# Optimization experiments

Measured on AMD Instinct MI355X. Metric: run time of the kernel, lower is better.

## Reference

```python
import jax, jax.numpy as jnp
import numpy as np

D_MODEL, NUM_HEADS, D_HEAD = 1024, 16, 64
B, T = 2, 2048


def setup_inputs() -> dict:
    key = jax.random.key(0)
    ks = jax.random.split(key, 9)
    s_in = 1.0 / np.sqrt(D_MODEL)
    s_proj = 1.0 / np.sqrt(NUM_HEADS * D_HEAD)
    x = jax.random.normal(ks[0], (B, T, D_MODEL), dtype=jnp.float32)
    # stacked per-head projection weights (nn.Linear: y = x @ W.T + b -> store as [H, C, d_head])
    Wq = jax.random.uniform(ks[1], (NUM_HEADS, D_MODEL, D_HEAD), jnp.float32, -s_in, s_in)
    Wk = jax.random.uniform(ks[2], (NUM_HEADS, D_MODEL, D_HEAD), jnp.float32, -s_in, s_in)
    Wv = jax.random.uniform(ks[3], (NUM_HEADS, D_MODEL, D_HEAD), jnp.float32, -s_in, s_in)
    bq = jax.random.uniform(ks[4], (NUM_HEADS, D_HEAD), jnp.float32, -s_in, s_in)
    bk = jax.random.uniform(ks[5], (NUM_HEADS, D_HEAD), jnp.float32, -s_in, s_in)
    bv = jax.random.uniform(ks[6], (NUM_HEADS, D_HEAD), jnp.float32, -s_in, s_in)
    Wo = jax.random.uniform(ks[7], (NUM_HEADS * D_HEAD, D_MODEL), jnp.float32, -s_proj, s_proj)
    bo = jax.random.uniform(ks[8], (D_MODEL,), jnp.float32, -s_proj, s_proj)
    return {"x": x, "Wq": Wq, "Wk": Wk, "Wv": Wv, "bq": bq, "bk": bk, "bv": bv, "Wo": Wo, "bo": bo}


def reference(x, Wq, Wk, Wv, bq, bk, bv, Wo, bo):
    Bsz, Tlen, C = x.shape
    # per-head projections, vectorized over heads: [B, H, T, d_head]
    q = jnp.einsum('btc,hcd->bhtd', x, Wq) + bq[None, :, None, :]
    k = jnp.einsum('btc,hcd->bhtd', x, Wk) + bk[None, :, None, :]
    v = jnp.einsum('btc,hcd->bhtd', x, Wv) + bv[None, :, None, :]
    # NOTE: source scales by sqrt(C) = sqrt(d_model), not sqrt(d_head); no causal mask
    scores = jnp.einsum('bhtd,bhsd->bhts', q, k) / jnp.sqrt(jnp.asarray(C, x.dtype))
    attn = jax.nn.softmax(scores, axis=-1)
    out = jnp.einsum('bhts,bhsd->bhtd', attn, v)  # [B, H, T, d_head]
    # concat heads along feature dim: [B, T, H*d_head]
    out = jnp.transpose(out, (0, 2, 1, 3)).reshape(Bsz, Tlen, -1)
    return out @ Wo + bo
```

## Files before the change

kernel.cpp:

```cpp
#include <hip/hip_runtime.h>

typedef __bf16 bf16;
typedef __bf16 bf16x4 __attribute__((ext_vector_type(4)));
typedef __bf16 bf16x8 __attribute__((ext_vector_type(8)));
typedef float  f32x4  __attribute__((ext_vector_type(4)));

#define T_SEQ  2048
#define NHEAD  16
#define DHEAD  64
#define DMODEL 1024
#define MTOT   4096
#define L2E    1.4426950408889634f

static __device__ __forceinline__ f32x4 mfma16(bf16x8 a, bf16x8 b, f32x4 c) {
    return __builtin_amdgcn_mfma_f32_16x16x32_bf16(a, b, c, 0, 0, 0);
}

__global__ __launch_bounds__(256) void prep(
    const float* __restrict__ x,  bf16* __restrict__ xbf,
    const float* __restrict__ Wq, const float* __restrict__ Wk,
    const float* __restrict__ Wv, bf16* __restrict__ wt,
    const float* __restrict__ Wo, bf16* __restrict__ wot)
{
    __shared__ float t[64][68];
    const int bid = blockIdx.x, tid = threadIdx.x;

    if (bid < 2048) {
        const int i = bid * 256 + tid;
        const float4 a = ((const float4*)x)[i * 2];
        const float4 b = ((const float4*)x)[i * 2 + 1];
        bf16x8 v;
        v[0] = (bf16)a.x; v[1] = (bf16)a.y; v[2] = (bf16)a.z; v[3] = (bf16)a.w;
        v[4] = (bf16)b.x; v[5] = (bf16)b.y; v[6] = (bf16)b.z; v[7] = (bf16)b.w;
        ((bf16x8*)xbf)[i] = v;
        return;
    }

    const float* in; bf16* out;
    int R, Cc; long ib, ob; int r0, c0;
    if (bid < 2816) {
        int b2 = bid - 2048;
        int w = b2 >> 8, rem = b2 & 255;
        int rt = rem & 15, head = rem >> 4;
        in  = (w == 0 ? Wq : w == 1 ? Wk : Wv);
        out = wt + (size_t)w * 1024 * 1024;
        R = 1024; Cc = 64;
        ib = (long)head * 65536; ob = (long)head * 65536;
        r0 = rt * 64; c0 = 0;
    } else {
        int b3 = bid - 2816;
        in = Wo; out = wot;
        R = 1024; Cc = 1024;
        ib = 0; ob = 0;
        r0 = (b3 & 15) * 64; c0 = (b3 >> 4) * 64;
    }

#pragma unroll
    for (int i = 0; i < 4; ++i) {
        int idx = i * 256 + tid;
        int row = idx >> 4, cb = (idx & 15) * 4;
        float4 v = *(const float4*)&in[ib + (long)(r0 + row) * Cc + c0 + cb];
        t[row][cb + 0] = v.x; t[row][cb + 1] = v.y;
        t[row][cb + 2] = v.z; t[row][cb + 3] = v.w;
    }
    __syncthreads();
#pragma unroll
    for (int i = 0; i < 2; ++i) {
        int idx = i * 256 + tid;
        int row = idx >> 3, cb = (idx & 7) * 8;
        bf16x8 v;
#pragma unroll
        for (int j = 0; j < 8; ++j) v[j] = (bf16)t[cb + j][row];
        *(bf16x8*)&out[ob + (long)(c0 + row) * R + r0 + cb] = v;
    }
}

__global__ __launch_bounds__(256) void qkv_gemm(
    const bf16* __restrict__ x, const bf16* __restrict__ wt,
    const float* __restrict__ bq, const float* __restrict__ bk,
    const float* __restrict__ bv,
    bf16* __restrict__ qws, bf16* __restrict__ kws, bf16* __restrict__ vtws)
{
    __shared__ __align__(16) bf16 xs[128][72];
    __shared__ __align__(16) bf16 wsh[3][64][72];

    const int m0 = blockIdx.x * 128;
    const int h  = blockIdx.y;
    const int tid = threadIdx.x, wid = tid >> 6, lane = tid & 63;
    const int lr = lane & 15, lg = lane >> 4;

    const bf16* wbase[3];
#pragma unroll
    for (int w = 0; w < 3; ++w)
        wbase[w] = wt + ((size_t)(w * NHEAD + h)) * DHEAD * DMODEL;

    f32x4 acc[3][2][4];
#pragma unroll
    for (int w = 0; w < 3; ++w)
#pragma unroll
        for (int mi = 0; mi < 2; ++mi)
#pragma unroll
            for (int nt = 0; nt < 4; ++nt) acc[w][mi][nt] = (f32x4)0.0f;

    bf16x8 xr[4], wr[3][2];
#pragma unroll
    for (int i = 0; i < 4; ++i) {
        int idx = i * 256 + tid;
        int row = idx >> 3, cb = (idx & 7) * 8;
        xr[i] = *(const bf16x8*)&x[(size_t)(m0 + row) * DMODEL + cb];
    }
#pragma unroll
    for (int w = 0; w < 3; ++w)
#pragma unroll
        for (int i = 0; i < 2; ++i) {
            int idx = i * 256 + tid;
            int row = idx >> 3, cb = (idx & 7) * 8;
            wr[w][i] = *(const bf16x8*)&wbase[w][(size_t)row * DMODEL + cb];
        }

    for (int kt = 0; kt < 16; ++kt) {
        __syncthreads();
#pragma unroll
        for (int i = 0; i < 4; ++i) {
            int idx = i * 256 + tid;
            int row = idx >> 3, cb = (idx & 7) * 8;
            *(bf16x8*)&xs[row][cb] = xr[i];
        }
#pragma unroll
        for (int w = 0; w < 3; ++w)
#pragma unroll
            for (int i = 0; i < 2; ++i) {
                int idx = i * 256 + tid;
                int row = idx >> 3, cb = (idx & 7) * 8;
                *(bf16x8*)&wsh[w][row][cb] = wr[w][i];
            }
        __syncthreads();

        if (kt < 15) {
            const int kofs = (kt + 1) * 64;
#pragma unroll
            for (int i = 0; i < 4; ++i) {
                int idx = i * 256 + tid;
                int row = idx >> 3, cb = (idx & 7) * 8;
                xr[i] = *(const bf16x8*)&x[(size_t)(m0 + row) * DMODEL + kofs + cb];
            }
#pragma unroll
            for (int w = 0; w < 3; ++w)
#pragma unroll
                for (int i = 0; i < 2; ++i) {
                    int idx = i * 256 + tid;
                    int row = idx >> 3, cb = (idx & 7) * 8;
                    wr[w][i] = *(const bf16x8*)&wbase[w][(size_t)row * DMODEL + kofs + cb];
                }
        }

        bf16x8 af[2][2];
#pragma unroll
        for (int mi = 0; mi < 2; ++mi)
#pragma unroll
            for (int ks = 0; ks < 2; ++ks)
                af[mi][ks] = *(const bf16x8*)&xs[wid * 32 + mi * 16 + lr][ks * 32 + lg * 8];

#pragma unroll
        for (int w = 0; w < 3; ++w)
#pragma unroll
            for (int nt = 0; nt < 4; ++nt)
#pragma unroll
                for (int ks = 0; ks < 2; ++ks) {
                    bf16x8 bfr = *(const bf16x8*)&wsh[w][nt * 16 + lr][ks * 32 + lg * 8];
#pragma unroll
                    for (int mi = 0; mi < 2; ++mi)
                        acc[w][mi][nt] = mfma16(af[mi][ks], bfr, acc[w][mi][nt]);
                }
    }

    const float* bias[3] = { bq + h * DHEAD, bk + h * DHEAD, bv + h * DHEAD };
#pragma unroll
    for (int w = 0; w < 3; ++w)
#pragma unroll
        for (int nt = 0; nt < 4; ++nt) {
            int d = nt * 16 + lr;
            float bs = bias[w][d];
#pragma unroll
            for (int mi = 0; mi < 2; ++mi)
#pragma unroll
                for (int j = 0; j < 4; ++j) {
                    int mrow = m0 + wid * 32 + mi * 16 + lg * 4 + j;
                    int b = mrow >> 11, t = mrow & 2047;
                    float val = acc[w][mi][nt][j] + bs;
                    size_t bh = (size_t)b * NHEAD + h;
                    if (w == 0)
                        qws[(bh * T_SEQ + t) * DHEAD + d] = (bf16)val;
                    else if (w == 1)
                        kws[(bh * T_SEQ + t) * DHEAD + d] = (bf16)val;
                    else
                        vtws[(bh * DHEAD + d) * T_SEQ + t] = (bf16)val;
                }
        }
}

template<int S, bool PARTIAL>
__global__ __launch_bounds__(512, 4) void attn_split(
    const bf16* __restrict__ qws, const bf16* __restrict__ kws,
    const bf16* __restrict__ vtws,
    bf16* __restrict__ po, float* __restrict__ pml, bf16* __restrict__ aws)
{
    __shared__ __align__(16) bf16 kls[2][64][72];
    __shared__ __align__(16) bf16 vls[2][64][72];

    const int id = blockIdx.x;
    const int w  = (id & 7) * (32 * S) + (id >> 3);
    const int bh = w / (8 * S);
    const int rem = w - bh * (8 * S);
    const int qt = rem / S;
    const int sidx = rem - qt * S;
    const int t0 = (sidx * 32) / S, t1 = ((sidx + 1) * 32) / S;

    const int b = bh >> 4, h = bh & 15;
    const bf16* Q  = qws  + (size_t)bh * T_SEQ * DHEAD;
    const bf16* K  = kws  + (size_t)bh * T_SEQ * DHEAD;
    const bf16* Vt = vtws + (size_t)bh * DHEAD * T_SEQ;

    const int tid = threadIdx.x, wid = tid >> 6, lane = tid & 63;
    const int lr = lane & 15, lg = lane >> 4;

    const int srow = tid >> 3, scb = (tid & 7) * 8;
    const int sl = tid & 7;
    const int vcol = 32 * (sl >> 2) + 4 * (sl & 3);

    int q0[2];
    bf16x8 qf[2][2];
#pragma unroll
    for (int g = 0; g < 2; ++g) {
        q0[g] = qt * 256 + g * 128 + wid * 16;
#pragma unroll
        for (int ks = 0; ks < 2; ++ks) {
            bf16x8 v = *(const bf16x8*)&Q[(size_t)(q0[g] + lr) * DHEAD + ks * 32 + lg * 8];
#pragma unroll
            for (int j = 0; j < 8; ++j) v[j] = (bf16)((float)v[j] * 0.03125f);
            qf[g][ks] = v;
        }
    }

    f32x4 o[2][4];
#pragma unroll
    for (int g = 0; g < 2; ++g)
#pragma unroll
        for (int nt = 0; nt < 4; ++nt) o[g][nt] = (f32x4)0.0f;
    float mrun[2] = { -1e30f, -1e30f }, lrun[2] = { 0.f, 0.f };
    float m2c[2]  = { -1e30f * L2E, -1e30f * L2E };

    bf16x8 kr;
    bf16x4 va, vb;
    kr = *(const bf16x8*)&K[(size_t)(t0 * 64 + srow) * DHEAD + scb];
    va = *(const bf16x4*)&Vt[(size_t)srow * T_SEQ + t0 * 64 + vcol];
    vb = *(const bf16x4*)&Vt[(size_t)srow * T_SEQ + t0 * 64 + vcol + 16];
    *(bf16x8*)&kls[0][srow][scb] = kr;
    *(bf16x8*)&vls[0][srow][scb] = __builtin_shufflevector(va, vb, 0, 1, 2, 3, 4, 5, 6, 7);

    int cur = 0;
    for (int t = t0; t < t1; ++t) {
        __syncthreads();

        const bool more = (t + 1) < t1;
        if (more) {
            int kvn = (t + 1) * 64;
            kr = *(const bf16x8*)&K[(size_t)(kvn + srow) * DHEAD + scb];
            va = *(const bf16x4*)&Vt[(size_t)srow * T_SEQ + kvn + vcol];
            vb = *(const bf16x4*)&Vt[(size_t)srow * T_SEQ + kvn + vcol + 16];
        }

        f32x4 s[2][4];
        __builtin_amdgcn_s_setprio(1);
#pragma unroll
        for (int nt = 0; nt < 4; ++nt) {
            bf16x8 k0 = *(const bf16x8*)&kls[cur][nt * 16 + lr][0 + lg * 8];
            bf16x8 k1 = *(const bf16x8*)&kls[cur][nt * 16 + lr][32 + lg * 8];
#pragma unroll
            for (int g = 0; g < 2; ++g) {
                s[g][nt] = mfma16(k0, qf[g][0], (f32x4)0.0f);
                s[g][nt] = mfma16(k1, qf[g][1], s[g][nt]);
            }
        }
        __builtin_amdgcn_s_setprio(0);

        bf16x8 pf[2][2];
#pragma unroll
        for (int g = 0; g < 2; ++g) {
            float vm0 = fmaxf(fmaxf(s[g][0][0], s[g][0][1]), fmaxf(s[g][0][2], s[g][0][3]));
            float vm1 = fmaxf(fmaxf(s[g][1][0], s[g][1][1]), fmaxf(s[g][1][2], s[g][1][3]));
            float vm2 = fmaxf(fmaxf(s[g][2][0], s[g][2][1]), fmaxf(s[g][2][2], s[g][2][3]));
            float vm3 = fmaxf(fmaxf(s[g][3][0], s[g][3][1]), fmaxf(s[g][3][2], s[g][3][3]));
            float vm = fmaxf(fmaxf(vm0, vm1), fmaxf(vm2, vm3));

            const bool skip = __all(vm <= mrun[g] + 8.0f);
            if (!skip) {
                float vmr = fmaxf(vm, __shfl_xor(vm, 16));
                vmr = fmaxf(vmr, __shfl_xor(vmr, 32));
                float mnew = fmaxf(mrun[g], vmr);
                float alpha = __builtin_amdgcn_exp2f((mrun[g] - mnew) * L2E);
                lrun[g] *= alpha;
                mrun[g] = mnew;
                m2c[g] = mnew * L2E;
                float ab[4];
#pragma unroll
                for (int j = 0; j < 4; ++j) ab[j] = __shfl(alpha, lg * 4 + j);
#pragma unroll
                for (int nt = 0; nt < 4; ++nt)
#pragma unroll
                    for (int j = 0; j < 4; ++j) o[g][nt][j] *= ab[j];
            }

            const float m2 = m2c[g];
            float p[4][4];
            float rs = 0.f;
#pragma unroll
            for (int nt = 0; nt < 4; ++nt)
#pragma unroll
                for (int j = 0; j < 4; ++j) {
                    p[nt][j] = __builtin_amdgcn_exp2f(fmaf(s[g][nt][j], L2E, -m2));
                    rs += p[nt][j];
                }
            lrun[g] += rs;

#pragma unroll
            for (int ks = 0; ks < 2; ++ks) {
                bf16x8 pk;
#pragma unroll
                for (int j = 0; j < 4; ++j) {
                    pk[j]     = (bf16)p[2 * ks][j];
                    pk[j + 4] = (bf16)p[2 * ks + 1][j];
                }
                pf[g][ks] = pk;
            }
        }

        __builtin_amdgcn_s_setprio(1);
#pragma unroll
        for (int ks = 0; ks < 2; ++ks)
#pragma unroll
            for (int nt = 0; nt < 4; ++nt) {
                bf16x8 vf = *(const bf16x8*)&vls[cur][nt * 16 + lr][ks * 32 + lg * 8];
#pragma unroll
                for (int g = 0; g < 2; ++g)
                    o[g][nt] = mfma16(pf[g][ks], vf, o[g][nt]);
            }
        __builtin_amdgcn_s_setprio(0);

        if (more) {
            *(bf16x8*)&kls[cur ^ 1][srow][scb] = kr;
            *(bf16x8*)&vls[cur ^ 1][srow][scb] =
                __builtin_shufflevector(va, vb, 0, 1, 2, 3, 4, 5, 6, 7);
        }
        cur ^= 1;
    }

#pragma unroll
    for (int g = 0; g < 2; ++g) {
        float lrow = lrun[g];
        lrow += __shfl_xor(lrow, 16);
        lrow += __shfl_xor(lrow, 32);

        float linv[4];
#pragma unroll
        for (int j = 0; j < 4; ++j) linv[j] = 1.0f / __shfl(lrow, lg * 4 + j);

        if (PARTIAL) {
            const size_t pbase = (size_t)(sidx * 32 + bh) * T_SEQ * DHEAD;
#pragma unroll
            for (int nt = 0; nt < 4; ++nt) {
                int dcol = nt * 16 + lr;
#pragma unroll
                for (int j = 0; j < 4; ++j) {
                    int tq = q0[g] + lg * 4 + j;
                    po[pbase + (size_t)tq * DHEAD + dcol] = (bf16)(o[g][nt][j] * linv[j]);
                }
            }
            if (lg == 0) {
                size_t mlidx = ((size_t)(sidx * 32 + bh) * T_SEQ + (q0[g] + lr)) * 2;
                pml[mlidx]     = mrun[g];
                pml[mlidx + 1] = lrow;
            }
        } else {
            const size_t obase = ((size_t)b * T_SEQ) * DMODEL + (size_t)h * DHEAD;
#pragma unroll
            for (int nt = 0; nt < 4; ++nt) {
                int dcol = nt * 16 + lr;
#pragma unroll
                for (int j = 0; j < 4; ++j) {
                    int tq = q0[g] + lg * 4 + j;
                    aws[obase + (size_t)tq * DMODEL + dcol] = (bf16)(o[g][nt][j] * linv[j]);
                }
            }
        }
    }
}

template<int S>
__global__ __launch_bounds__(256) void attn_combine(
    const bf16* __restrict__ po, const float* __restrict__ pml,
    bf16* __restrict__ aws)
{
    const int g = blockIdx.x * 256 + threadIdx.x;
    const int r = g >> 3, dblk = g & 7;
    const int bh = r >> 11, tq = r & 2047;

    float ms[S], ls[S];
    float m = -1e30f;
#pragma unroll
    for (int s = 0; s < S; ++s) {
        float2 v = ((const float2*)pml)[(size_t)(s * 32 + bh) * T_SEQ + tq];
        ms[s] = v.x; ls[s] = v.y;
        m = fmaxf(m, ms[s]);
    }
    float L = 0.f, wgt[S];
#pragma unroll
    for (int s = 0; s < S; ++s) {
        wgt[s] = ls[s] * __builtin_amdgcn_exp2f((ms[s] - m) * L2E);
        L += wgt[s];
    }
    float inv = 1.0f / L;

    float acc[8];
#pragma unroll
    for (int j = 0; j < 8; ++j) acc[j] = 0.f;
#pragma unroll
    for (int s = 0; s < S; ++s) {
        bf16x8 ov = *(const bf16x8*)&po[((size_t)(s * 32 + bh) * T_SEQ + tq) * DHEAD + dblk * 8];
        float c = wgt[s] * inv;
#pragma unroll
        for (int j = 0; j < 8; ++j) acc[j] = fmaf(c, (float)ov[j], acc[j]);
    }
    bf16x8 out;
#pragma unroll
    for (int j = 0; j < 8; ++j) out[j] = (bf16)acc[j];

    const int b = bh >> 4, h = bh & 15;
    *(bf16x8*)&aws[((size_t)(b * T_SEQ + tq)) * DMODEL + h * DHEAD + dblk * 8] = out;
}

__global__ __launch_bounds__(256) void out_gemm(
    const bf16* __restrict__ a, const bf16* __restrict__ wot,
    const float* __restrict__ bo, float* __restrict__ out)
{
    __shared__ __align__(16) bf16 as[128][72];
    __shared__ __align__(16) bf16 wsh[128][72];

    const int m0 = blockIdx.x * 128, n0 = blockIdx.y * 128;
    const int tid = threadIdx.x, wid = tid >> 6, lane = tid & 63;
    const int lr = lane & 15, lg = lane >> 4;

    f32x4 acc[2][8];
#pragma unroll
    for (int mi = 0; mi < 2; ++mi)
#pragma unroll
        for (int nt = 0; nt < 8; ++nt) acc[mi][nt] = (f32x4)0.0f;

    bf16x8 ar[4], wr[4];
#pragma unroll
    for (int i = 0; i < 4; ++i) {
        int idx = i * 256 + tid;
        int row = idx >> 3, cb = (idx & 7) * 8;
        ar[i] = *(const bf16x8*)&a[(size_t)(m0 + row) * DMODEL + cb];
        wr[i] = *(const bf16x8*)&wot[(size_t)(n0 + row) * DMODEL + cb];
    }

    for (int kt = 0; kt < 16; ++kt) {
        __syncthreads();
#pragma unroll
        for (int i = 0; i < 4; ++i) {
            int idx = i * 256 + tid;
            int row = idx >> 3, cb = (idx & 7) * 8;
            *(bf16x8*)&as[row][cb]  = ar[i];
            *(bf16x8*)&wsh[row][cb] = wr[i];
        }
        __syncthreads();

        if (kt < 15) {
            const int kofs = (kt + 1) * 64;
#pragma unroll
            for (int i = 0; i < 4; ++i) {
                int idx = i * 256 + tid;
                int row = idx >> 3, cb = (idx & 7) * 8;
                ar[i] = *(const bf16x8*)&a[(size_t)(m0 + row) * DMODEL + kofs + cb];
                wr[i] = *(const bf16x8*)&wot[(size_t)(n0 + row) * DMODEL + kofs + cb];
            }
        }

        bf16x8 af[2][2];
#pragma unroll
        for (int mi = 0; mi < 2; ++mi)
#pragma unroll
            for (int ks = 0; ks < 2; ++ks)
                af[mi][ks] = *(const bf16x8*)&as[wid * 32 + mi * 16 + lr][ks * 32 + lg * 8];

#pragma unroll
        for (int nt = 0; nt < 8; ++nt)
#pragma unroll
            for (int ks = 0; ks < 2; ++ks) {
                bf16x8 bfr = *(const bf16x8*)&wsh[nt * 16 + lr][ks * 32 + lg * 8];
#pragma unroll
                for (int mi = 0; mi < 2; ++mi)
                    acc[mi][nt] = mfma16(af[mi][ks], bfr, acc[mi][nt]);
            }
    }

#pragma unroll
    for (int nt = 0; nt < 8; ++nt) {
        int n = n0 + nt * 16 + lr;
        float bs = bo[n];
#pragma unroll
        for (int mi = 0; mi < 2; ++mi)
#pragma unroll
            for (int j = 0; j < 4; ++j) {
                int m = m0 + wid * 32 + mi * 16 + lg * 4 + j;
                out[(size_t)m * DMODEL + n] = acc[mi][nt][j] + bs;
            }
    }
}

extern "C" void kernel_launch(void* const* d_in, const int* in_sizes, int n_in,
                              void* d_out, int out_size, void* d_ws, size_t ws_size,
                              hipStream_t stream)
{
    const float* x  = (const float*)d_in[0];
    const float* Wq = (const float*)d_in[1];
    const float* Wk = (const float*)d_in[2];
    const float* Wv = (const float*)d_in[3];
    const float* bq = (const float*)d_in[4];
    const float* bk = (const float*)d_in[5];
    const float* bv = (const float*)d_in[6];
    const float* Wo = (const float*)d_in[7];
    const float* bo = (const float*)d_in[8];
    float* out = (float*)d_out;

    const size_t M1 = (size_t)1024 * 1024;
    bf16* ws   = (bf16*)d_ws;
    bf16* xbf  = ws;
    bf16* qws  = ws + 4 * M1;
    bf16* kws  = qws + 4 * M1;
    bf16* vtws = kws + 4 * M1;
    bf16* wt   = vtws + 4 * M1;
    bf16* wot  = wt + 3 * M1;
    bf16* aws  = xbf;
    bf16* po   = wot + 1 * M1;

    const size_t BASE = 20 * M1 * 2;
    const size_t PER  = 4 * M1 * 2 + (size_t)65536 * 2 * 4;

    dim3 tb(256);
    prep<<<dim3(3072), tb, 0, stream>>>(x, xbf, Wq, Wk, Wv, wt, Wo, wot);
    qkv_gemm<<<dim3(MTOT / 128, NHEAD), tb, 0, stream>>>(xbf, wt, bq, bk, bv, qws, kws, vtws);

    if (ws_size >= BASE + 2 * PER) {
        float* pml = (float*)(po + 2 * 4 * M1);
        attn_split<2, true><<<dim3(512), dim3(512), 0, stream>>>(qws, kws, vtws, po, pml, aws);
        attn_combine<2><<<dim3(2048), tb, 0, stream>>>(po, pml, aws);
    } else {
        attn_split<1, false><<<dim3(256), dim3(512), 0, stream>>>(qws, kws, vtws, po, nullptr, aws);
    }

    out_gemm<<<dim3(MTOT / 128, DMODEL / 128), tb, 0, stream>>>(aws, wot, bo, out);
}
```

Measured before the change: 117.4 us.

## Compute softmax row sums via MFMA and shrink out-projection GEMM M-tile

In the attention kernel, the softmax denominator is now accumulated with an extra MFMA of the probability fragments against a ones vector. This replaces per-lane scalar adds and the cross-lane shuffle reductions, and the row sum arrives already in the output layout. The output-projection GEMM tile shrinks from 128 to 64 rows per block, doubling the block count to improve occupancy and CU coverage, at the cost of more weight-tile reloads. The MFMA-based sum adds matrix work per KV tile and accumulates from bf16-rounded probabilities.

```diff
diff --git a/kernel.cpp b/kernel.cpp
--- a/kernel.cpp
+++ b/kernel.cpp
@@ -228,6 +228,10 @@
     const int sl = tid & 7;
     const int vcol = 32 * (sl >> 2) + 4 * (sl & 3);
 
+    bf16x8 onesf;
+#pragma unroll
+    for (int j = 0; j < 8; ++j) onesf[j] = (bf16)1.0f;
+
     int q0[2];
     bf16x8 qf[2][2];
 #pragma unroll
@@ -242,12 +246,14 @@
         }
     }
 
-    f32x4 o[2][4];
-#pragma unroll
-    for (int g = 0; g < 2; ++g)
+    f32x4 o[2][4], lsum[2];
+#pragma unroll
+    for (int g = 0; g < 2; ++g) {
 #pragma unroll
         for (int nt = 0; nt < 4; ++nt) o[g][nt] = (f32x4)0.0f;
-    float mrun[2] = { -1e30f, -1e30f }, lrun[2] = { 0.f, 0.f };
+        lsum[g] = (f32x4)0.0f;
+    }
+    float mrun[2] = { -1e30f, -1e30f };
     float m2c[2]  = { -1e30f * L2E, -1e30f * L2E };
 
     bf16x8 kr;
@@ -299,13 +305,14 @@
                 vmr = fmaxf(vmr, __shfl_xor(vmr, 32));
                 float mnew = fmaxf(mrun[g], vmr);
                 float alpha = __builtin_amdgcn_exp2f((mrun[g] - mnew) * L2E);
-                lrun[g] *= alpha;
                 mrun[g] = mnew;
                 m2c[g] = mnew * L2E;
                 float ab[4];
 #pragma unroll
                 for (int j = 0; j < 4; ++j) ab[j] = __shfl(alpha, lg * 4 + j);
 #pragma unroll
+                for (int j = 0; j < 4; ++j) lsum[g][j] *= ab[j];
+#pragma unroll
                 for (int nt = 0; nt < 4; ++nt)
 #pragma unroll
                     for (int j = 0; j < 4; ++j) o[g][nt][j] *= ab[j];
@@ -313,15 +320,11 @@
 
             const float m2 = m2c[g];
             float p[4][4];
-            float rs = 0.f;
 #pragma unroll
             for (int nt = 0; nt < 4; ++nt)
 #pragma unroll
-                for (int j = 0; j < 4; ++j) {
+                for (int j = 0; j < 4; ++j)
                     p[nt][j] = __builtin_amdgcn_exp2f(fmaf(s[g][nt][j], L2E, -m2));
-                    rs += p[nt][j];
-                }
-            lrun[g] += rs;
 
 #pragma unroll
             for (int ks = 0; ks < 2; ++ks) {
@@ -337,7 +340,10 @@
 
         __builtin_amdgcn_s_setprio(1);
 #pragma unroll
-        for (int ks = 0; ks < 2; ++ks)
+        for (int ks = 0; ks < 2; ++ks) {
+#pragma unroll
+            for (int g = 0; g < 2; ++g)
+                lsum[g] = mfma16(pf[g][ks], onesf, lsum[g]);
 #pragma unroll
             for (int nt = 0; nt < 4; ++nt) {
                 bf16x8 vf = *(const bf16x8*)&vls[cur][nt * 16 + lr][ks * 32 + lg * 8];
@@ -345,6 +351,7 @@
                 for (int g = 0; g < 2; ++g)
                     o[g][nt] = mfma16(pf[g][ks], vf, o[g][nt]);
             }
+        }
         __builtin_amdgcn_s_setprio(0);
 
         if (more) {
@@ -357,13 +364,9 @@
 
 #pragma unroll
     for (int g = 0; g < 2; ++g) {
-        float lrow = lrun[g];
-        lrow += __shfl_xor(lrow, 16);
-        lrow += __shfl_xor(lrow, 32);
-
         float linv[4];
 #pragma unroll
-        for (int j = 0; j < 4; ++j) linv[j] = 1.0f / __shfl(lrow, lg * 4 + j);
+        for (int j = 0; j < 4; ++j) linv[j] = 1.0f / lsum[g][j];
 
         if (PARTIAL) {
             const size_t pbase = (size_t)(sidx * 32 + bh) * T_SEQ * DHEAD;
@@ -376,10 +379,18 @@
                     po[pbase + (size_t)tq * DHEAD + dcol] = (bf16)(o[g][nt][j] * linv[j]);
                 }
             }
-            if (lg == 0) {
-                size_t mlidx = ((size_t)(sidx * 32 + bh) * T_SEQ + (q0[g] + lr)) * 2;
-                pml[mlidx]     = mrun[g];
-                pml[mlidx + 1] = lrow;
+            {
+                int js = lr & 3;
+                float wv = lsum[g][0];
+                wv = (js == 1) ? lsum[g][1] : wv;
+                wv = (js == 2) ? lsum[g][2] : wv;
+                wv = (js == 3) ? lsum[g][3] : wv;
+                float lrow_q = __shfl(wv, 16 * (lr >> 2) + (lr & 3));
+                if (lg == 0) {
+                    size_t mlidx = ((size_t)(sidx * 32 + bh) * T_SEQ + (q0[g] + lr)) * 2;
+                    pml[mlidx]     = mrun[g];
+                    pml[mlidx + 1] = lrow_q;
+                }
             }
         } else {
             const size_t obase = ((size_t)b * T_SEQ) * DMODEL + (size_t)h * DHEAD;
@@ -443,65 +454,74 @@
     const bf16* __restrict__ a, const bf16* __restrict__ wot,
     const float* __restrict__ bo, float* __restrict__ out)
 {
-    __shared__ __align__(16) bf16 as[128][72];
+    __shared__ __align__(16) bf16 as[64][72];
     __shared__ __align__(16) bf16 wsh[128][72];
 
-    const int m0 = blockIdx.x * 128, n0 = blockIdx.y * 128;
+    const int m0 = blockIdx.x * 64, n0 = blockIdx.y * 128;
     const int tid = threadIdx.x, wid = tid >> 6, lane = tid & 63;
     const int lr = lane & 15, lg = lane >> 4;
 
-    f32x4 acc[2][8];
-#pragma unroll
-    for (int mi = 0; mi < 2; ++mi)
-#pragma unroll
-        for (int nt = 0; nt < 8; ++nt) acc[mi][nt] = (f32x4)0.0f;
-
-    bf16x8 ar[4], wr[4];
+    f32x4 acc[8];
+#pragma unroll
+    for (int nt = 0; nt < 8; ++nt) acc[nt] = (f32x4)0.0f;
+
+    bf16x8 ar[2], wr[4];
+#pragma unroll
+    for (int i = 0; i < 2; ++i) {
+        int idx = i * 256 + tid;
+        int row = idx >> 3, cb = (idx & 7) * 8;
+        ar[i] = *(const bf16x8*)&a[(size_t)(m0 + row) * DMODEL + cb];
+    }
 #pragma unroll
     for (int i = 0; i < 4; ++i) {
         int idx = i * 256 + tid;
         int row = idx >> 3, cb = (idx & 7) * 8;
-        ar[i] = *(const bf16x8*)&a[(size_t)(m0 + row) * DMODEL + cb];
         wr[i] = *(const bf16x8*)&wot[(size_t)(n0 + row) * DMODEL + cb];
     }
 
     for (int kt = 0; kt < 16; ++kt) {
         __syncthreads();
+#pragma unroll
+        for (int i = 0; i < 2; ++i) {
+            int idx = i * 256 + tid;
+            int row = idx >> 3, cb = (idx & 7) * 8;
+            *(bf16x8*)&as[row][cb] = ar[i];
+        }
 #pragma unroll
         for (int i = 0; i < 4; ++i) {
             int idx = i * 256 + tid;
             int row = idx >> 3, cb = (idx & 7) * 8;
-            *(bf16x8*)&as[row][cb]  = ar[i];
             *(bf16x8*)&wsh[row][cb] = wr[i];
         }
         __syncthreads();
 
         if (kt < 15) {
             const int kofs = (kt + 1) * 64;
+#pragma unroll
+            for (int i = 0; i < 2; ++i) {
+                int idx = i * 256 + tid;
+                int row = idx >> 3, cb = (idx & 7) * 8;
+                ar[i] = *(const bf16x8*)&a[(size_t)(m0 + row) * DMODEL + kofs + cb];
+            }
 #pragma unroll
             for (int i = 0; i < 4; ++i) {
                 int idx = i * 256 + tid;
                 int row = idx >> 3, cb = (idx & 7) * 8;
-                ar[i] = *(const bf16x8*)&a[(size_t)(m0 + row) * DMODEL + kofs + cb];
                 wr[i] = *(const bf16x8*)&wot[(size_t)(n0 + row) * DMODEL + kofs + cb];
             }
         }
 
-        bf16x8 af[2][2];
-#pragma unroll
-        for (int mi = 0; mi < 2; ++mi)
-#pragma unroll
-            for (int ks = 0; ks < 2; ++ks)
-                af[mi][ks] = *(const bf16x8*)&as[wid * 32 + mi * 16 + lr][ks * 32 + lg * 8];
+        bf16x8 af[2];
+#pragma unroll
+        for (int ks = 0; ks < 2; ++ks)
+            af[ks] = *(const bf16x8*)&as[wid * 16 + lr][ks * 32 + lg * 8];
 
 #pragma unroll
         for (int nt = 0; nt < 8; ++nt)
 #pragma unroll
             for (int ks = 0; ks < 2; ++ks) {
                 bf16x8 bfr = *(const bf16x8*)&wsh[nt * 16 + lr][ks * 32 + lg * 8];
-#pragma unroll
-                for (int mi = 0; mi < 2; ++mi)
-                    acc[mi][nt] = mfma16(af[mi][ks], bfr, acc[mi][nt]);
+                acc[nt] = mfma16(af[ks], bfr, acc[nt]);
             }
     }
 
@@ -510,12 +530,10 @@
         int n = n0 + nt * 16 + lr;
         float bs = bo[n];
 #pragma unroll
-        for (int mi = 0; mi < 2; ++mi)
-#pragma unroll
-            for (int j = 0; j < 4; ++j) {
-                int m = m0 + wid * 32 + mi * 16 + lg * 4 + j;
-                out[(size_t)m * DMODEL + n] = acc[mi][nt][j] + bs;
-            }
+        for (int j = 0; j < 4; ++j) {
+            int m = m0 + wid * 16 + lg * 4 + j;
+            out[(size_t)m * DMODEL + n] = acc[nt][j] + bs;
+        }
     }
 }
 
@@ -560,5 +578,5 @@
         attn_split<1, false><<<dim3(256), dim3(512), 0, stream>>>(qws, kws, vtws, po, nullptr, aws);
     }
 
-    out_gemm<<<dim3(MTOT / 128, DMODEL / 128), tb, 0, stream>>>(aws, wot, bo, out);
-}
+    out_gemm<<<dim3(MTOT / 64, DMODEL / 128), tb, 0, stream>>>(aws, wot, bo, out);
+}
```

Result: no change. 115.9 us (-1.3%).
